# Optimization experiments

Hardware: AMD Instinct MI355X
Metric: run time of the kernel (lower is better)

## Reference

```python
import jax, jax.numpy as jnp
import numpy as np

B = 16384
IMG = 28          # MNIST side
K = 3             # conv kernel side
OUT = IMG - K + 1 # 26, valid convolution
HID = 512
NCLS = 10


def setup_inputs() -> dict:
    key = jax.random.key(0)
    k0, k1, k2, k3 = jax.random.split(key, 4)
    x = jax.random.normal(k0, (B, IMG * IMG), dtype=jnp.float32)
    conv_w = jax.random.normal(k1, (K, K), dtype=jnp.float32) * 0.1
    W1 = jax.random.normal(k2, (OUT * OUT, HID), dtype=jnp.float32) * 0.04
    b1 = jnp.zeros((HID,), dtype=jnp.float32)
    W2 = jax.random.normal(k3, (HID, NCLS), dtype=jnp.float32) * 0.04
    b2 = jnp.zeros((NCLS,), dtype=jnp.float32)
    return {"x": x, "conv_w": conv_w, "W1": W1, "b1": b1, "W2": W2, "b2": b2}


def reference(x, conv_w, W1, b1, W2, b2):
    # x: [B, 784] -> [B, 1, 28, 28]
    img = x.reshape(-1, 1, IMG, IMG)
    kern = conv_w.reshape(1, 1, K, K)  # OIHW
    # Valid cross-correlation (matches per-window tensordot in the torch code),
    # one fused batched conv instead of Python loops over positions/samples.
    y = jax.lax.conv_general_dilated(
        img, kern, window_strides=(1, 1), padding="VALID",
        dimension_numbers=("NCHW", "OIHW", "NCHW"))  # [B, 1, 26, 26]
    h = y.reshape(y.shape[0], OUT * OUT)               # flatten(start_dim=1)
    h = jax.nn.relu(h @ W1 + b1)                       # hidden layer
    logits = h @ W2 + b2                               # [B, 10]
    return logits
```

## Files before the change

### kernel.cpp

```cpp
#include <hip/hip_runtime.h>
#include <stdint.h>

#define NCLS 10
#define HID  512
#define KP   800
#define NKK  25
#define BM   32
#define THREADS 512
#define NBLK 512
#define YSTR 808
#define HSTR 520

typedef __attribute__((ext_vector_type(8))) short short8;
typedef __attribute__((ext_vector_type(4))) float f32x4;

__device__ __forceinline__ unsigned short f2bf(float f) {
  union { float f; unsigned u; } v; v.f = f;
  unsigned r = v.u + 0x7fffu + ((v.u >> 16) & 1u);
  return (unsigned short)(r >> 16);
}
#define PK2(a, b) ((unsigned)f2bf(a) | ((unsigned)f2bf(b) << 16))

__global__ void prep_kernel(const float* __restrict__ W1, const float* __restrict__ cw,
                            const float* __restrict__ W2,
                            unsigned short* __restrict__ Wf, unsigned short* __restrict__ W2f) {
  int i = blockIdx.x * blockDim.x + threadIdx.x;
  const int total1 = KP * HID;
  if (i < total1) {
    int k = i >> 9, n = i & 511;
    float s = 0.f;
    if (k < 784) {
      int iy = k / 28, ix = k - iy * 28;
#pragma unroll
      for (int ky = 0; ky < 3; ++ky) {
        int oy = iy - ky;
        if ((unsigned)oy < 26u) {
#pragma unroll
          for (int kx = 0; kx < 3; ++kx) {
            int ox = ix - kx;
            if ((unsigned)ox < 26u)
              s += cw[ky * 3 + kx] * W1[(oy * 26 + ox) * HID + n];
          }
        }
      }
    }
    int dst = (((k >> 5) * 32 + (n >> 4)) * 64 + ((k >> 3) & 3) * 16 + (n & 15)) * 8 + (k & 7);
    Wf[dst] = f2bf(s);
  } else if (i < total1 + 8192) {
    int i2 = i - total1;
    int k = i2 >> 4, n = i2 & 15;
    unsigned short v = 0;
    if (n < NCLS) v = f2bf(W2[k * NCLS + n]);
    int dst = ((k >> 5) * 64 + ((k >> 3) & 3) * 16 + n) * 8 + (k & 7);
    W2f[dst] = v;
  }
}

__global__ __launch_bounds__(THREADS, 4)
void main_kernel(const float* __restrict__ x, const unsigned short* __restrict__ Wf,
                 const float* __restrict__ b1, const unsigned short* __restrict__ W2f,
                 const float* __restrict__ b2, float* __restrict__ out) {
  __shared__ __align__(16) unsigned short y_lds[BM * YSTR];
  __shared__ float part_lds[16 * 256];

  const int tid  = threadIdx.x;
  const int lane = tid & 63;
  const int w    = tid >> 6;
  const int r0   = blockIdx.x * BM;
  const int row  = lane & 15;
  const int kg   = lane >> 4;
  const int wcol = w * 64;

  for (int c = tid; c < BM * 98; c += THREADS) {
    int r  = c / 98;
    int kc = c - r * 98;
    const f32x4* p = (const f32x4*)(x + (size_t)(r0 + r) * 784 + kc * 8);
    f32x4 v0 = p[0], v1 = p[1];
    uint4 d;
    d.x = PK2(v0[0], v0[1]); d.y = PK2(v0[2], v0[3]);
    d.z = PK2(v1[0], v1[1]); d.w = PK2(v1[2], v1[3]);
    *(uint4*)&y_lds[r * YSTR + kc * 8] = d;
  }
  if (tid < BM * 2) {
    int r = tid >> 1, hf = tid & 1;
    uint4 z; z.x = z.y = z.z = z.w = 0u;
    *(uint4*)&y_lds[r * YSTR + 784 + hf * 8] = z;
  }
  __syncthreads();

  f32x4 acc1[2][4];
#pragma unroll
  for (int rt = 0; rt < 2; ++rt)
#pragma unroll
    for (int ct = 0; ct < 4; ++ct)
      acc1[rt][ct] = (f32x4){0.f, 0.f, 0.f, 0.f};

#pragma unroll
  for (int kk = 0; kk < NKK; ++kk) {
    short8 bb[4], a[2];
#pragma unroll
    for (int ct = 0; ct < 4; ++ct)
      bb[ct] = *(const short8*)(Wf + ((size_t)((kk * 32 + w * 4 + ct) * 64) + lane) * 8);
#pragma unroll
    for (int rt = 0; rt < 2; ++rt)
      a[rt] = *(const short8*)&y_lds[(rt * 16 + row) * YSTR + kk * 32 + kg * 8];
#pragma unroll
    for (int rt = 0; rt < 2; ++rt)
#pragma unroll
      for (int ct = 0; ct < 4; ++ct)
        acc1[rt][ct] = __builtin_amdgcn_mfma_f32_16x16x32_bf16(a[rt], bb[ct], acc1[rt][ct], 0, 0, 0);
  }
  __syncthreads();

  unsigned short* h_lds = y_lds;
  float b1v[4];
#pragma unroll
  for (int ct = 0; ct < 4; ++ct)
    b1v[ct] = b1[wcol + ct * 16 + row];

#pragma unroll
  for (int rt = 0; rt < 2; ++rt)
#pragma unroll
    for (int ct = 0; ct < 4; ++ct)
#pragma unroll
      for (int j = 0; j < 4; ++j) {
        int rr = rt * 16 + kg * 4 + j;
        int cc = wcol + ct * 16 + row;
        float hv = acc1[rt][ct][j] + b1v[ct];
        hv = hv > 0.f ? hv : 0.f;
        h_lds[rr * HSTR + cc] = f2bf(hv);
      }
  __syncthreads();

  {
    short8 b0  = *(const short8*)(W2f + ((size_t)(2 * w) * 64 + lane) * 8);
    short8 b1f = *(const short8*)(W2f + ((size_t)(2 * w + 1) * 64 + lane) * 8);
#pragma unroll
    for (int rt = 0; rt < 2; ++rt) {
      short8 a0 = *(const short8*)&h_lds[(rt * 16 + row) * HSTR + w * 64 + kg * 8];
      short8 a1 = *(const short8*)&h_lds[(rt * 16 + row) * HSTR + w * 64 + 32 + kg * 8];
      f32x4 p = (f32x4){0.f, 0.f, 0.f, 0.f};
      p = __builtin_amdgcn_mfma_f32_16x16x32_bf16(a0, b0, p, 0, 0, 0);
      p = __builtin_amdgcn_mfma_f32_16x16x32_bf16(a1, b1f, p, 0, 0, 0);
#pragma unroll
      for (int j = 0; j < 4; ++j)
        part_lds[(w * 2 + rt) * 256 + (kg * 4 + j) * 16 + row] = p[j];
    }
  }
  __syncthreads();

  for (int o = tid; o < BM * NCLS; o += THREADS) {
    int r  = o / NCLS;
    int cc = o - r * NCLS;
    float s = b2[cc];
#pragma unroll
    for (int w8 = 0; w8 < 8; ++w8)
      s += part_lds[(w8 * 2 + (r >> 4)) * 256 + (r & 15) * 16 + cc];
    out[(size_t)(r0 + r) * NCLS + cc] = s;
  }
}

extern "C" void kernel_launch(void* const* d_in, const int* in_sizes, int n_in,
                              void* d_out, int out_size, void* d_ws, size_t ws_size,
                              hipStream_t stream) {
  const float* x  = (const float*)d_in[0];
  const float* cw = (const float*)d_in[1];
  const float* W1 = (const float*)d_in[2];
  const float* b1 = (const float*)d_in[3];
  const float* W2 = (const float*)d_in[4];
  const float* b2 = (const float*)d_in[5];
  float* out = (float*)d_out;

  unsigned short* Wf  = (unsigned short*)d_ws;
  unsigned short* W2f = (unsigned short*)((char*)d_ws + 819200);

  prep_kernel<<<1632, 256, 0, stream>>>(W1, cw, W2, Wf, W2f);
  main_kernel<<<NBLK, THREADS, 0, stream>>>(x, Wf, b1, W2f, b2, out);
}
```

Baseline: 33.75 us.

## Warp-specialize input loading and double the row tile to overlap loads with MFMA

Doubles the batch tile to 64 rows, so each block reuses every fused conv+W1 weight fragment across twice as many rows, and halves the grid to 256 blocks. Adds four producer warps that convert later chunks of the input rows to bf16 into LDS while eight consumer warps run MFMAs on earlier chunks. The K loop is split into four stages separated by barriers. The larger LDS footprint (about 135KB) limits each CU to one block. The extra barriers and producer warps that sit idle during compute may offset the overlap gained.

```diff
diff --git a/kernel.cpp b/kernel.cpp
--- a/kernel.cpp
+++ b/kernel.cpp
@@ -4,10 +4,9 @@
 #define NCLS 10
 #define HID  512
 #define KP   800
-#define NKK  25
-#define BM   32
-#define THREADS 512
-#define NBLK 512
+#define BM   64
+#define THREADS 768
+#define NBLK 256
 #define YSTR 808
 #define HSTR 520
 
@@ -56,12 +55,12 @@
   }
 }
 
-__global__ __launch_bounds__(THREADS, 4)
+__global__ __launch_bounds__(THREADS, 3)
 void main_kernel(const float* __restrict__ x, const unsigned short* __restrict__ Wf,
                  const float* __restrict__ b1, const unsigned short* __restrict__ W2f,
                  const float* __restrict__ b2, float* __restrict__ out) {
   __shared__ __align__(16) unsigned short y_lds[BM * YSTR];
-  __shared__ float part_lds[16 * 256];
+  __shared__ float part_lds[32 * 256];
 
   const int tid  = threadIdx.x;
   const int lane = tid & 63;
@@ -71,15 +70,14 @@
   const int kg   = lane >> 4;
   const int wcol = w * 64;
 
-  for (int c = tid; c < BM * 98; c += THREADS) {
-    int r  = c / 98;
-    int kc = c - r * 98;
-    const f32x4* p = (const f32x4*)(x + (size_t)(r0 + r) * 784 + kc * 8);
+  for (int u = tid; u < BM * 28; u += THREADS) {
+    int r = u / 28, j = u - r * 28;
+    const f32x4* p = (const f32x4*)(x + (size_t)(r0 + r) * 784 + j * 8);
     f32x4 v0 = p[0], v1 = p[1];
     uint4 d;
     d.x = PK2(v0[0], v0[1]); d.y = PK2(v0[2], v0[3]);
     d.z = PK2(v1[0], v1[1]); d.w = PK2(v1[2], v1[3]);
-    *(uint4*)&y_lds[r * YSTR + kc * 8] = d;
+    *(uint4*)&y_lds[r * YSTR + j * 8] = d;
   }
   if (tid < BM * 2) {
     int r = tid >> 1, hf = tid & 1;
@@ -88,55 +86,73 @@
   }
   __syncthreads();
 
-  f32x4 acc1[2][4];
+  f32x4 acc1[4][4];
 #pragma unroll
-  for (int rt = 0; rt < 2; ++rt)
+  for (int rt = 0; rt < 4; ++rt)
 #pragma unroll
     for (int ct = 0; ct < 4; ++ct)
       acc1[rt][ct] = (f32x4){0.f, 0.f, 0.f, 0.f};
 
 #pragma unroll
-  for (int kk = 0; kk < NKK; ++kk) {
-    short8 bb[4], a[2];
+  for (int c = 0; c < 4; ++c) {
+    if (w < 8) {
+      const int kkS = (c == 0) ? 0 : (c == 1) ? 7 : (c == 2) ? 13 : 19;
+      const int kkE = (c == 0) ? 7 : (c == 1) ? 13 : (c == 2) ? 19 : 25;
+#pragma unroll
+      for (int kk = kkS; kk < kkE; ++kk) {
+        short8 bb[4], a[4];
+#pragma unroll
+        for (int ct = 0; ct < 4; ++ct)
+          bb[ct] = *(const short8*)(Wf + ((size_t)((kk * 32 + w * 4 + ct) * 64) + lane) * 8);
+#pragma unroll
+        for (int rt = 0; rt < 4; ++rt)
+          a[rt] = *(const short8*)&y_lds[(rt * 16 + row) * YSTR + kk * 32 + kg * 8];
+#pragma unroll
+        for (int rt = 0; rt < 4; ++rt)
+#pragma unroll
+          for (int ct = 0; ct < 4; ++ct)
+            acc1[rt][ct] = __builtin_amdgcn_mfma_f32_16x16x32_bf16(a[rt], bb[ct], acc1[rt][ct], 0, 0, 0);
+      }
+    } else if (c < 3) {
+      const int k0  = (c == 0) ? 224 : (c == 1) ? 416 : 608;
+      const int upr = (c == 2) ? 22 : 24;
+      for (int u = tid - 512; u < BM * upr; u += 256) {
+        int r = u / upr, j = u - r * upr;
+        const f32x4* p = (const f32x4*)(x + (size_t)(r0 + r) * 784 + k0 + j * 8);
+        f32x4 v0 = p[0], v1 = p[1];
+        uint4 d;
+        d.x = PK2(v0[0], v0[1]); d.y = PK2(v0[2], v0[3]);
+        d.z = PK2(v1[0], v1[1]); d.w = PK2(v1[2], v1[3]);
+        *(uint4*)&y_lds[r * YSTR + k0 + j * 8] = d;
+      }
+    }
+    __syncthreads();
+  }
+
+  if (w < 8) {
+    unsigned short* h_lds = y_lds;
+    float b1v[4];
 #pragma unroll
     for (int ct = 0; ct < 4; ++ct)
-      bb[ct] = *(const short8*)(Wf + ((size_t)((kk * 32 + w * 4 + ct) * 64) + lane) * 8);
+      b1v[ct] = b1[wcol + ct * 16 + row];
+
 #pragma unroll
-    for (int rt = 0; rt < 2; ++rt)
-      a[rt] = *(const short8*)&y_lds[(rt * 16 + row) * YSTR + kk * 32 + kg * 8];
-#pragma unroll
-    for (int rt = 0; rt < 2; ++rt)
+    for (int rt = 0; rt < 4; ++rt)
 #pragma unroll
       for (int ct = 0; ct < 4; ++ct)
-        acc1[rt][ct] = __builtin_amdgcn_mfma_f32_16x16x32_bf16(a[rt], bb[ct], acc1[rt][ct], 0, 0, 0);
-  }
-  __syncthreads();
+#pragma unroll
+        for (int j = 0; j < 4; ++j) {
+          int rr = rt * 16 + kg * 4 + j;
+          int cc = wcol + ct * 16 + row;
+          float hv = acc1[rt][ct][j] + b1v[ct];
+          hv = hv > 0.f ? hv : 0.f;
+          h_lds[rr * HSTR + cc] = f2bf(hv);
+        }
 
-  unsigned short* h_lds = y_lds;
-  float b1v[4];
-#pragma unroll
-  for (int ct = 0; ct < 4; ++ct)
-    b1v[ct] = b1[wcol + ct * 16 + row];
-
-#pragma unroll
-  for (int rt = 0; rt < 2; ++rt)
-#pragma unroll
-    for (int ct = 0; ct < 4; ++ct)
-#pragma unroll
-      for (int j = 0; j < 4; ++j) {
-        int rr = rt * 16 + kg * 4 + j;
-        int cc = wcol + ct * 16 + row;
-        float hv = acc1[rt][ct][j] + b1v[ct];
-        hv = hv > 0.f ? hv : 0.f;
-        h_lds[rr * HSTR + cc] = f2bf(hv);
-      }
-  __syncthreads();
-
-  {
     short8 b0  = *(const short8*)(W2f + ((size_t)(2 * w) * 64 + lane) * 8);
     short8 b1f = *(const short8*)(W2f + ((size_t)(2 * w + 1) * 64 + lane) * 8);
 #pragma unroll
-    for (int rt = 0; rt < 2; ++rt) {
+    for (int rt = 0; rt < 4; ++rt) {
       short8 a0 = *(const short8*)&h_lds[(rt * 16 + row) * HSTR + w * 64 + kg * 8];
       short8 a1 = *(const short8*)&h_lds[(rt * 16 + row) * HSTR + w * 64 + 32 + kg * 8];
       f32x4 p = (f32x4){0.f, 0.f, 0.f, 0.f};
@@ -144,18 +160,18 @@
       p = __builtin_amdgcn_mfma_f32_16x16x32_bf16(a1, b1f, p, 0, 0, 0);
 #pragma unroll
       for (int j = 0; j < 4; ++j)
-        part_lds[(w * 2 + rt) * 256 + (kg * 4 + j) * 16 + row] = p[j];
+        part_lds[(w * 4 + rt) * 256 + (kg * 4 + j) * 16 + row] = p[j];
     }
   }
   __syncthreads();
 
-  for (int o = tid; o < BM * NCLS; o += THREADS) {
-    int r  = o / NCLS;
-    int cc = o - r * NCLS;
+  if (tid < BM * NCLS) {
+    int r  = tid / NCLS;
+    int cc = tid - r * NCLS;
     float s = b2[cc];
 #pragma unroll
     for (int w8 = 0; w8 < 8; ++w8)
-      s += part_lds[(w8 * 2 + (r >> 4)) * 256 + (r & 15) * 16 + cc];
+      s += part_lds[(w8 * 4 + (r >> 4)) * 256 + (r & 15) * 16 + cc];
     out[(size_t)(r0 + r) * NCLS + cc] = s;
   }
 }
```

Measured after the change: 28.66 us. -15.1%, faster.
